# Kernel optimization log

Measured on AMD Instinct MI355X. Metric: run time of the kernel, lower is better.

## Reference

```python
import jax, jax.numpy as jnp
import numpy as np

N_NODES = 100000
N_EDGES = 300000
D = 128
HID = 128

def setup_inputs() -> dict:
    key = jax.random.key(0)
    ks = jax.random.split(key, 12)
    s = lambda fan_in: 1.0 / np.sqrt(fan_in)
    return {
        "user_emb": jax.random.normal(ks[0], (N_NODES, D), jnp.float32),
        "item_emb": jax.random.normal(ks[1], (N_NODES, D), jnp.float32),
        "ei_ui": jax.random.randint(ks[2], (2, N_EDGES), 0, N_NODES, jnp.int64),
        "ei_iu": jax.random.randint(ks[3], (2, N_EDGES), 0, N_NODES, jnp.int64),
        "W_bi_ui": jax.random.normal(ks[4], (2 * D, HID), jnp.float32) * s(2 * D),
        "b_bi_ui": jnp.zeros((HID,), jnp.float32),
        "W1_ui": jax.random.normal(ks[5], (HID, HID), jnp.float32) * s(HID),
        "b1_ui": jnp.zeros((HID,), jnp.float32),
        "W2_ui": jax.random.normal(ks[6], (HID, 1), jnp.float32) * s(HID),
        "b2_ui": jnp.zeros((1,), jnp.float32),
        "W_bi_iu": jax.random.normal(ks[7], (2 * D, HID), jnp.float32) * s(2 * D),
        "b_bi_iu": jnp.zeros((HID,), jnp.float32),
        "W1_iu": jax.random.normal(ks[8], (HID, HID), jnp.float32) * s(HID),
        "b1_iu": jnp.zeros((HID,), jnp.float32),
        "W2_iu": jax.random.normal(ks[9], (HID, 1), jnp.float32) * s(HID),
        "b2_iu": jnp.zeros((1,), jnp.float32),
    }

def _decode_edge_type(src_emb, dst_emb, edge_index, W_bi, b_bi, W1, b1, W2, b2):
    # gather endpoint embeddings and concat -> [E, 2D]
    e = jnp.concatenate([src_emb[edge_index[0]], dst_emb[edge_index[1]]], axis=1)
    h = jax.nn.elu(e @ W_bi + b_bi)          # bilinear -> ELU
    h = jax.nn.elu(h @ W1 + b1)              # linear1 -> ELU
    p = jax.nn.sigmoid(h @ W2 + b2)          # linear2 -> sigmoid
    return p.reshape(-1)                     # [E]

def reference(user_emb, item_emb, ei_ui, ei_iu,
              W_bi_ui, b_bi_ui, W1_ui, b1_ui, W2_ui, b2_ui,
              W_bi_iu, b_bi_iu, W1_iu, b1_iu, W2_iu, b2_iu):
    # edge type (user, clicks, item): source=user, target=item
    p_ui = _decode_edge_type(user_emb, item_emb, ei_ui,
                             W_bi_ui, b_bi_ui, W1_ui, b1_ui, W2_ui, b2_ui)
    # edge type (item, clicked_by, user): source=item, target=user
    p_iu = _decode_edge_type(item_emb, user_emb, ei_iu,
                             W_bi_iu, b_bi_iu, W1_iu, b1_iu, W2_iu, b2_iu)
    return jnp.stack([p_ui, p_iu])  # [2, E]
```

## Files before the change

kernel.cpp:

```cpp
#include <hip/hip_runtime.h>

typedef __attribute__((ext_vector_type(8))) short short8;
typedef __attribute__((ext_vector_type(4))) float float4v;
typedef __attribute__((ext_vector_type(4))) int int4v;

#define E_EDGES 300000
#define EPB 64
#define NBLK ((E_EDGES + EPB - 1) / EPB)
#define TAB_ELEMS 12800000

__device__ __forceinline__ short f2bf(float f) {
    unsigned u = __float_as_uint(f);
    return (short)((u + 0x7FFFu + ((u >> 16) & 1u)) >> 16);
}
__device__ __forceinline__ unsigned pk_bf16(float a, float b) {
    unsigned ua = __float_as_uint(a), ub = __float_as_uint(b);
    ua += 0x7FFFu + ((ua >> 16) & 1u);
    ub += 0x7FFFu + ((ub >> 16) & 1u);
    return __builtin_amdgcn_perm(ub, ua, 0x07060302);
}

__device__ __forceinline__ void cp16(const void* g, void* l) {
    __builtin_amdgcn_global_load_lds(
        (const __attribute__((address_space(1))) unsigned int*)g,
        (__attribute__((address_space(3))) unsigned int*)l, 16, 0, 0);
}

__global__ void prep_weights(const float* __restrict__ Wbi_ui, const float* __restrict__ W1_ui,
                             const float* __restrict__ Wbi_iu, const float* __restrict__ W1_iu,
                             short* __restrict__ ws) {
    __shared__ short tr[64 * 68];
    const int t = blockIdx.y;
    const int m = blockIdx.x;
    const float* W; int k0, n0, obase;
    if (m < 8) {
        int kt = m >> 1, nh = m & 1;
        W = t ? Wbi_iu : Wbi_ui; k0 = kt * 64; n0 = nh * 64;
        obase = t * 32768 + kt * 8192;
    } else {
        int mm = m - 8; int kt = mm >> 1, nh = mm & 1;
        W = t ? W1_iu : W1_ui; k0 = kt * 64; n0 = nh * 64;
        obase = 65536 + t * 16384 + kt * 8192;
    }
    const int tid = threadIdx.x;
    for (int it = 0; it < 16; ++it) {
        int flat = it * 256 + tid;
        int kk = flat >> 6, nn = flat & 63;
        tr[nn * 68 + kk] = f2bf(W[(size_t)(k0 + kk) * 128 + n0 + nn]);
    }
    __syncthreads();
    for (int it = 0; it < 16; ++it) {
        int flat = it * 256 + tid;
        int nn = flat >> 6, kk = flat & 63;
        int n = n0 + nn;
        ws[obase + n * 64 + (kk ^ ((n & 7) << 3))] = tr[nn * 68 + kk];
    }
}

__global__ void cvt_tables(const float* __restrict__ ue, const float* __restrict__ ie,
                           short* __restrict__ tab) {
    const float* src = blockIdx.y ? ie : ue;
    short* dst = tab + (size_t)blockIdx.y * TAB_ELEMS;
    const int stride = gridDim.x * blockDim.x;
    for (int g = blockIdx.x * blockDim.x + threadIdx.x; g < TAB_ELEMS / 8; g += stride) {
        const float* p = src + (size_t)g * 8;
        float4v v0 = ((const float4v*)p)[0];
        float4v v1 = ((const float4v*)p)[1];
        int4v w = { (int)pk_bf16(v0[0], v0[1]), (int)pk_bf16(v0[2], v0[3]),
                    (int)pk_bf16(v1[0], v1[1]), (int)pk_bf16(v1[2], v1[3]) };
        *(int4v*)(dst + (size_t)g * 8) = w;
    }
}

template<bool BF16G>
__launch_bounds__(256, 4)
__global__ void edge_decoder(
    const float* __restrict__ user_emb, const float* __restrict__ item_emb,
    const int* __restrict__ ei_ui, const int* __restrict__ ei_iu,
    const float* __restrict__ b_bi_ui, const float* __restrict__ b1_ui,
    const float* __restrict__ W2_ui, const float* __restrict__ b2_ui,
    const float* __restrict__ b_bi_iu, const float* __restrict__ b1_iu,
    const float* __restrict__ W2_iu, const float* __restrict__ b2_iu,
    const short* __restrict__ ws, const short* __restrict__ tab,
    float* __restrict__ out)
{
    __shared__ short Blds[128 * 64];
    __shared__ short Hlds[4 * 16 * 136];

    const int type = blockIdx.y;
    const int e0 = blockIdx.x * EPB;
    const int tid = threadIdx.x;
    const int wave = tid >> 6, lane = tid & 63;
    const int q = lane >> 4, ln = lane & 15;

    const int*   ei   = type ? ei_iu : ei_ui;
    const float* bbi  = type ? b_bi_iu : b_bi_ui;
    const float* b1v  = type ? b1_iu : b1_ui;
    const float* W2v  = type ? W2_iu : W2_ui;
    const float* b2v  = type ? b2_iu : b2_ui;
    const short* WbiT = ws + type * 32768;
    const short* W1T  = ws + 65536 + type * 16384;

    const int erow = e0 + wave * 16 + ln;
    const int safe = (erow < E_EDGES) ? erow : 0;
    const int si = ei[safe];
    const int di = ei[E_EDGES + safe];

    for (int c = 0; c < 4; ++c)
        cp16(WbiT + c * 2048 + tid * 8, Blds + c * 2048 + tid * 8);

    short8 a[8];
    if (BF16G) {
        const short* sp = tab + (size_t)(type ? TAB_ELEMS : 0) + (size_t)si * 128;
        const short* dp = tab + (size_t)(type ? 0 : TAB_ELEMS) + (size_t)di * 128;
        for (int ks = 0; ks < 4; ++ks)
            a[ks] = *(const short8*)(sp + ks * 32 + q * 8);
        for (int ks = 4; ks < 8; ++ks)
            a[ks] = *(const short8*)(dp + (ks - 4) * 32 + q * 8);
    } else {
        const float* srcT = type ? item_emb : user_emb;
        const float* dstT = type ? user_emb : item_emb;
        for (int ks = 0; ks < 8; ++ks) {
            const float* p = (ks < 4) ? (srcT + (size_t)si * 128 + ks * 32 + q * 8)
                                      : (dstT + (size_t)di * 128 + (ks - 4) * 32 + q * 8);
            float4v v0 = ((const float4v*)p)[0];
            float4v v1 = ((const float4v*)p)[1];
            int4v w = { (int)pk_bf16(v0[0], v0[1]), (int)pk_bf16(v0[2], v0[3]),
                        (int)pk_bf16(v1[0], v1[1]), (int)pk_bf16(v1[2], v1[3]) };
            a[ks] = *(short8*)&w;
        }
    }

    float4v acc[8];
    for (int nt = 0; nt < 8; ++nt) acc[nt] = (float4v){0.f, 0.f, 0.f, 0.f};

    const int swz = (ln & 7) << 3;

    for (int kt = 0; kt < 4; ++kt) {
        __syncthreads();
        for (int ks2 = 0; ks2 < 2; ++ks2) {
            int ka = (ks2 * 32 + q * 8) ^ swz;
            for (int nt = 0; nt < 8; ++nt) {
                short8 bf = *(const short8*)&Blds[(nt * 16 + ln) * 64 + ka];
                acc[nt] = __builtin_amdgcn_mfma_f32_16x16x32_bf16(a[kt * 2 + ks2], bf, acc[nt], 0, 0, 0);
            }
        }
        __syncthreads();
        const short* nxt = (kt < 3) ? (WbiT + (kt + 1) * 8192) : W1T;
        for (int c = 0; c < 4; ++c)
            cp16(nxt + c * 2048 + tid * 8, Blds + c * 2048 + tid * 8);
    }

    short* Hw = Hlds + wave * (16 * 136);
    for (int nt = 0; nt < 8; ++nt) {
        int col = nt * 16 + ln;
        float bb = bbi[col];
        float4v v = acc[nt];
        for (int r = 0; r < 4; ++r) {
            float x = v[r] + bb;
            float h = x > 0.f ? x : (__expf(x) - 1.f);
            Hw[(q * 4 + r) * 136 + col] = f2bf(h);
        }
    }
    short8 a2[4];
    for (int ks = 0; ks < 4; ++ks)
        a2[ks] = *(const short8*)&Hw[ln * 136 + ks * 32 + q * 8];

    for (int nt = 0; nt < 8; ++nt) acc[nt] = (float4v){0.f, 0.f, 0.f, 0.f};

    for (int kt = 0; kt < 2; ++kt) {
        __syncthreads();
        for (int ks2 = 0; ks2 < 2; ++ks2) {
            int ka = (ks2 * 32 + q * 8) ^ swz;
            for (int nt = 0; nt < 8; ++nt) {
                short8 bf = *(const short8*)&Blds[(nt * 16 + ln) * 64 + ka];
                acc[nt] = __builtin_amdgcn_mfma_f32_16x16x32_bf16(a2[kt * 2 + ks2], bf, acc[nt], 0, 0, 0);
            }
        }
        __syncthreads();
        if (kt == 0)
            for (int c = 0; c < 4; ++c)
                cp16(W1T + 8192 + c * 2048 + tid * 8, Blds + c * 2048 + tid * 8);
    }

    float s0 = 0.f, s1 = 0.f, s2 = 0.f, s3 = 0.f;
    for (int nt = 0; nt < 8; ++nt) {
        int col = nt * 16 + ln;
        float bb = b1v[col], wv = W2v[col];
        float4v v = acc[nt];
        float x;
        x = v[0] + bb; x = x > 0.f ? x : (__expf(x) - 1.f); s0 += x * wv;
        x = v[1] + bb; x = x > 0.f ? x : (__expf(x) - 1.f); s1 += x * wv;
        x = v[2] + bb; x = x > 0.f ? x : (__expf(x) - 1.f); s2 += x * wv;
        x = v[3] + bb; x = x > 0.f ? x : (__expf(x) - 1.f); s3 += x * wv;
    }
    for (int off = 1; off < 16; off <<= 1) {
        s0 += __shfl_xor(s0, off);
        s1 += __shfl_xor(s1, off);
        s2 += __shfl_xor(s2, off);
        s3 += __shfl_xor(s3, off);
    }
    if (ln < 4) {
        float sv = (ln == 0) ? s0 : (ln == 1) ? s1 : (ln == 2) ? s2 : s3;
        int e = e0 + wave * 16 + q * 4 + ln;
        if (e < E_EDGES) {
            float z = sv + b2v[0];
            out[type * E_EDGES + e] = 1.f / (1.f + __expf(-z));
        }
    }
}

extern "C" void kernel_launch(void* const* d_in, const int* in_sizes, int n_in,
                              void* d_out, int out_size, void* d_ws, size_t ws_size,
                              hipStream_t stream) {
    const float* user_emb = (const float*)d_in[0];
    const float* item_emb = (const float*)d_in[1];
    const int*   ei_ui    = (const int*)d_in[2];
    const int*   ei_iu    = (const int*)d_in[3];
    const float* W_bi_ui  = (const float*)d_in[4];
    const float* b_bi_ui  = (const float*)d_in[5];
    const float* W1_ui    = (const float*)d_in[6];
    const float* b1_ui    = (const float*)d_in[7];
    const float* W2_ui    = (const float*)d_in[8];
    const float* b2_ui    = (const float*)d_in[9];
    const float* W_bi_iu  = (const float*)d_in[10];
    const float* b_bi_iu  = (const float*)d_in[11];
    const float* W1_iu    = (const float*)d_in[12];
    const float* b1_iu    = (const float*)d_in[13];
    const float* W2_iu    = (const float*)d_in[14];
    const float* b2_iu    = (const float*)d_in[15];
    short* ws  = (short*)d_ws;
    short* tab = ws + 98304;
    float* out = (float*)d_out;

    const size_t need = 98304u * 2u + (size_t)2 * TAB_ELEMS * 2u;

    hipLaunchKernelGGL(prep_weights, dim3(12, 2), dim3(256), 0, stream,
                       W_bi_ui, W1_ui, W_bi_iu, W1_iu, ws);
    if (ws_size >= need) {
        hipLaunchKernelGGL(cvt_tables, dim3(1024, 2), dim3(256), 0, stream,
                           user_emb, item_emb, tab);
        edge_decoder<true><<<dim3(NBLK, 2), dim3(256), 0, stream>>>(
            user_emb, item_emb, ei_ui, ei_iu,
            b_bi_ui, b1_ui, W2_ui, b2_ui,
            b_bi_iu, b1_iu, W2_iu, b2_iu,
            ws, tab, out);
    } else {
        edge_decoder<false><<<dim3(NBLK, 2), dim3(256), 0, stream>>>(
            user_emb, item_emb, ei_ui, ei_iu,
            b_bi_ui, b1_ui, W2_ui, b2_ui,
            b_bi_iu, b1_iu, W2_iu, b2_iu,
            ws, tab, out);
    }
}
```

Baseline: 260.9 us.

## Process two 16-edge tiles per wave, fold biases into accumulators, merge prep kernels

Edges per block double to 128, so each wave computes two 16-row MFMA tiles. Every B fragment read from LDS is reused for both tiles, which halves LDS weight traffic and barriers per edge. Biases now seed the accumulators instead of being added in the epilogue. The weight-prep and table-conversion kernels become one launch. In exchange it needs more registers (launch bounds lowered to 3 blocks per CU) and a larger H staging buffer. The fallback path now also writes the bf16 tables into a workspace that may be too small for them.

```diff
diff --git a/kernel.cpp b/kernel.cpp
--- a/kernel.cpp
+++ b/kernel.cpp
@@ -5,7 +5,7 @@
 typedef __attribute__((ext_vector_type(4))) int int4v;
 
 #define E_EDGES 300000
-#define EPB 64
+#define EPB 128
 #define NBLK ((E_EDGES + EPB - 1) / EPB)
 #define TAB_ELEMS 12800000
 
@@ -19,19 +19,34 @@
     ub += 0x7FFFu + ((ub >> 16) & 1u);
     return __builtin_amdgcn_perm(ub, ua, 0x07060302);
 }
-
 __device__ __forceinline__ void cp16(const void* g, void* l) {
     __builtin_amdgcn_global_load_lds(
         (const __attribute__((address_space(1))) unsigned int*)g,
         (__attribute__((address_space(3))) unsigned int*)l, 16, 0, 0);
 }
 
-__global__ void prep_weights(const float* __restrict__ Wbi_ui, const float* __restrict__ W1_ui,
-                             const float* __restrict__ Wbi_iu, const float* __restrict__ W1_iu,
-                             short* __restrict__ ws) {
+__global__ void prep_all(const float* __restrict__ ue, const float* __restrict__ ie,
+                         const float* __restrict__ Wbi_ui, const float* __restrict__ W1_ui,
+                         const float* __restrict__ Wbi_iu, const float* __restrict__ W1_iu,
+                         short* __restrict__ ws) {
     __shared__ short tr[64 * 68];
     const int t = blockIdx.y;
-    const int m = blockIdx.x;
+    const int tid = threadIdx.x;
+    if (blockIdx.x < 1024) {
+        const float* src = t ? ie : ue;
+        short* dst = ws + 98304 + (size_t)t * TAB_ELEMS;
+        const int stride = 1024 * 256;
+        for (int g = blockIdx.x * 256 + tid; g < TAB_ELEMS / 8; g += stride) {
+            const float* p = src + (size_t)g * 8;
+            float4v v0 = ((const float4v*)p)[0];
+            float4v v1 = ((const float4v*)p)[1];
+            int4v w = { (int)pk_bf16(v0[0], v0[1]), (int)pk_bf16(v0[2], v0[3]),
+                        (int)pk_bf16(v1[0], v1[1]), (int)pk_bf16(v1[2], v1[3]) };
+            *(int4v*)(dst + (size_t)g * 8) = w;
+        }
+        return;
+    }
+    const int m = blockIdx.x - 1024;
     const float* W; int k0, n0, obase;
     if (m < 8) {
         int kt = m >> 1, nh = m & 1;
@@ -42,7 +57,6 @@
         W = t ? W1_iu : W1_ui; k0 = kt * 64; n0 = nh * 64;
         obase = 65536 + t * 16384 + kt * 8192;
     }
-    const int tid = threadIdx.x;
     for (int it = 0; it < 16; ++it) {
         int flat = it * 256 + tid;
         int kk = flat >> 6, nn = flat & 63;
@@ -57,23 +71,8 @@
     }
 }
 
-__global__ void cvt_tables(const float* __restrict__ ue, const float* __restrict__ ie,
-                           short* __restrict__ tab) {
-    const float* src = blockIdx.y ? ie : ue;
-    short* dst = tab + (size_t)blockIdx.y * TAB_ELEMS;
-    const int stride = gridDim.x * blockDim.x;
-    for (int g = blockIdx.x * blockDim.x + threadIdx.x; g < TAB_ELEMS / 8; g += stride) {
-        const float* p = src + (size_t)g * 8;
-        float4v v0 = ((const float4v*)p)[0];
-        float4v v1 = ((const float4v*)p)[1];
-        int4v w = { (int)pk_bf16(v0[0], v0[1]), (int)pk_bf16(v0[2], v0[3]),
-                    (int)pk_bf16(v1[0], v1[1]), (int)pk_bf16(v1[2], v1[3]) };
-        *(int4v*)(dst + (size_t)g * 8) = w;
-    }
-}
-
 template<bool BF16G>
-__launch_bounds__(256, 4)
+__launch_bounds__(256, 3)
 __global__ void edge_decoder(
     const float* __restrict__ user_emb, const float* __restrict__ item_emb,
     const int* __restrict__ ei_ui, const int* __restrict__ ei_iu,
@@ -85,7 +84,7 @@
     float* __restrict__ out)
 {
     __shared__ short Blds[128 * 64];
-    __shared__ short Hlds[4 * 16 * 136];
+    __shared__ short Hlds[4 * 32 * 136];
 
     const int type = blockIdx.y;
     const int e0 = blockIdx.x * EPB;
@@ -101,38 +100,48 @@
     const short* WbiT = ws + type * 32768;
     const short* W1T  = ws + 65536 + type * 16384;
 
-    const int erow = e0 + wave * 16 + ln;
-    const int safe = (erow < E_EDGES) ? erow : 0;
-    const int si = ei[safe];
-    const int di = ei[E_EDGES + safe];
+    int si[2], di[2];
+    for (int mt = 0; mt < 2; ++mt) {
+        int erow = e0 + wave * 32 + mt * 16 + ln;
+        int safe = (erow < E_EDGES) ? erow : 0;
+        si[mt] = ei[safe];
+        di[mt] = ei[E_EDGES + safe];
+    }
 
     for (int c = 0; c < 4; ++c)
         cp16(WbiT + c * 2048 + tid * 8, Blds + c * 2048 + tid * 8);
 
-    short8 a[8];
+    short8 a[2][8];
     if (BF16G) {
-        const short* sp = tab + (size_t)(type ? TAB_ELEMS : 0) + (size_t)si * 128;
-        const short* dp = tab + (size_t)(type ? 0 : TAB_ELEMS) + (size_t)di * 128;
-        for (int ks = 0; ks < 4; ++ks)
-            a[ks] = *(const short8*)(sp + ks * 32 + q * 8);
-        for (int ks = 4; ks < 8; ++ks)
-            a[ks] = *(const short8*)(dp + (ks - 4) * 32 + q * 8);
+        for (int mt = 0; mt < 2; ++mt) {
+            const short* sp = tab + (size_t)(type ? TAB_ELEMS : 0) + (size_t)si[mt] * 128;
+            const short* dp = tab + (size_t)(type ? 0 : TAB_ELEMS) + (size_t)di[mt] * 128;
+            for (int ks = 0; ks < 4; ++ks)
+                a[mt][ks] = *(const short8*)(sp + ks * 32 + q * 8);
+            for (int ks = 4; ks < 8; ++ks)
+                a[mt][ks] = *(const short8*)(dp + (ks - 4) * 32 + q * 8);
+        }
     } else {
         const float* srcT = type ? item_emb : user_emb;
         const float* dstT = type ? user_emb : item_emb;
-        for (int ks = 0; ks < 8; ++ks) {
-            const float* p = (ks < 4) ? (srcT + (size_t)si * 128 + ks * 32 + q * 8)
-                                      : (dstT + (size_t)di * 128 + (ks - 4) * 32 + q * 8);
-            float4v v0 = ((const float4v*)p)[0];
-            float4v v1 = ((const float4v*)p)[1];
-            int4v w = { (int)pk_bf16(v0[0], v0[1]), (int)pk_bf16(v0[2], v0[3]),
-                        (int)pk_bf16(v1[0], v1[1]), (int)pk_bf16(v1[2], v1[3]) };
-            a[ks] = *(short8*)&w;
-        }
-    }
-
-    float4v acc[8];
-    for (int nt = 0; nt < 8; ++nt) acc[nt] = (float4v){0.f, 0.f, 0.f, 0.f};
+        for (int mt = 0; mt < 2; ++mt)
+            for (int ks = 0; ks < 8; ++ks) {
+                const float* p = (ks < 4) ? (srcT + (size_t)si[mt] * 128 + ks * 32 + q * 8)
+                                          : (dstT + (size_t)di[mt] * 128 + (ks - 4) * 32 + q * 8);
+                float4v v0 = ((const float4v*)p)[0];
+                float4v v1 = ((const float4v*)p)[1];
+                int4v w = { (int)pk_bf16(v0[0], v0[1]), (int)pk_bf16(v0[2], v0[3]),
+                            (int)pk_bf16(v1[0], v1[1]), (int)pk_bf16(v1[2], v1[3]) };
+                a[mt][ks] = *(short8*)&w;
+            }
+    }
+
+    float4v acc[2][8];
+    for (int nt = 0; nt < 8; ++nt) {
+        float bb = bbi[nt * 16 + ln];
+        acc[0][nt] = (float4v){bb, bb, bb, bb};
+        acc[1][nt] = acc[0][nt];
+    }
 
     const int swz = (ln & 7) << 3;
 
@@ -140,9 +149,11 @@
         __syncthreads();
         for (int ks2 = 0; ks2 < 2; ++ks2) {
             int ka = (ks2 * 32 + q * 8) ^ swz;
+            int ks = kt * 2 + ks2;
             for (int nt = 0; nt < 8; ++nt) {
                 short8 bf = *(const short8*)&Blds[(nt * 16 + ln) * 64 + ka];
-                acc[nt] = __builtin_amdgcn_mfma_f32_16x16x32_bf16(a[kt * 2 + ks2], bf, acc[nt], 0, 0, 0);
+                acc[0][nt] = __builtin_amdgcn_mfma_f32_16x16x32_bf16(a[0][ks], bf, acc[0][nt], 0, 0, 0);
+                acc[1][nt] = __builtin_amdgcn_mfma_f32_16x16x32_bf16(a[1][ks], bf, acc[1][nt], 0, 0, 0);
             }
         }
         __syncthreads();
@@ -151,30 +162,37 @@
             cp16(nxt + c * 2048 + tid * 8, Blds + c * 2048 + tid * 8);
     }
 
-    short* Hw = Hlds + wave * (16 * 136);
+    short* Hw = Hlds + wave * (32 * 136);
+    for (int mt = 0; mt < 2; ++mt)
+        for (int nt = 0; nt < 8; ++nt) {
+            int col = nt * 16 + ln;
+            float4v v = acc[mt][nt];
+            for (int r = 0; r < 4; ++r) {
+                float x = v[r];
+                float h = x > 0.f ? x : (__expf(x) - 1.f);
+                Hw[(mt * 16 + q * 4 + r) * 136 + col] = f2bf(h);
+            }
+        }
+    short8 a2[2][4];
+    for (int mt = 0; mt < 2; ++mt)
+        for (int ks = 0; ks < 4; ++ks)
+            a2[mt][ks] = *(const short8*)&Hw[(mt * 16 + ln) * 136 + ks * 32 + q * 8];
+
     for (int nt = 0; nt < 8; ++nt) {
-        int col = nt * 16 + ln;
-        float bb = bbi[col];
-        float4v v = acc[nt];
-        for (int r = 0; r < 4; ++r) {
-            float x = v[r] + bb;
-            float h = x > 0.f ? x : (__expf(x) - 1.f);
-            Hw[(q * 4 + r) * 136 + col] = f2bf(h);
-        }
-    }
-    short8 a2[4];
-    for (int ks = 0; ks < 4; ++ks)
-        a2[ks] = *(const short8*)&Hw[ln * 136 + ks * 32 + q * 8];
-
-    for (int nt = 0; nt < 8; ++nt) acc[nt] = (float4v){0.f, 0.f, 0.f, 0.f};
+        float bb = b1v[nt * 16 + ln];
+        acc[0][nt] = (float4v){bb, bb, bb, bb};
+        acc[1][nt] = acc[0][nt];
+    }
 
     for (int kt = 0; kt < 2; ++kt) {
         __syncthreads();
         for (int ks2 = 0; ks2 < 2; ++ks2) {
             int ka = (ks2 * 32 + q * 8) ^ swz;
+            int ks = kt * 2 + ks2;
             for (int nt = 0; nt < 8; ++nt) {
                 short8 bf = *(const short8*)&Blds[(nt * 16 + ln) * 64 + ka];
-                acc[nt] = __builtin_amdgcn_mfma_f32_16x16x32_bf16(a2[kt * 2 + ks2], bf, acc[nt], 0, 0, 0);
+                acc[0][nt] = __builtin_amdgcn_mfma_f32_16x16x32_bf16(a2[0][ks], bf, acc[0][nt], 0, 0, 0);
+                acc[1][nt] = __builtin_amdgcn_mfma_f32_16x16x32_bf16(a2[1][ks], bf, acc[1][nt], 0, 0, 0);
             }
         }
         __syncthreads();
@@ -183,29 +201,30 @@
                 cp16(W1T + 8192 + c * 2048 + tid * 8, Blds + c * 2048 + tid * 8);
     }
 
-    float s0 = 0.f, s1 = 0.f, s2 = 0.f, s3 = 0.f;
-    for (int nt = 0; nt < 8; ++nt) {
-        int col = nt * 16 + ln;
-        float bb = b1v[col], wv = W2v[col];
-        float4v v = acc[nt];
-        float x;
-        x = v[0] + bb; x = x > 0.f ? x : (__expf(x) - 1.f); s0 += x * wv;
-        x = v[1] + bb; x = x > 0.f ? x : (__expf(x) - 1.f); s1 += x * wv;
-        x = v[2] + bb; x = x > 0.f ? x : (__expf(x) - 1.f); s2 += x * wv;
-        x = v[3] + bb; x = x > 0.f ? x : (__expf(x) - 1.f); s3 += x * wv;
-    }
-    for (int off = 1; off < 16; off <<= 1) {
-        s0 += __shfl_xor(s0, off);
-        s1 += __shfl_xor(s1, off);
-        s2 += __shfl_xor(s2, off);
-        s3 += __shfl_xor(s3, off);
-    }
-    if (ln < 4) {
-        float sv = (ln == 0) ? s0 : (ln == 1) ? s1 : (ln == 2) ? s2 : s3;
-        int e = e0 + wave * 16 + q * 4 + ln;
-        if (e < E_EDGES) {
-            float z = sv + b2v[0];
-            out[type * E_EDGES + e] = 1.f / (1.f + __expf(-z));
+    for (int mt = 0; mt < 2; ++mt) {
+        float s0 = 0.f, s1 = 0.f, s2 = 0.f, s3 = 0.f;
+        for (int nt = 0; nt < 8; ++nt) {
+            float wv = W2v[nt * 16 + ln];
+            float4v v = acc[mt][nt];
+            float x;
+            x = v[0]; x = x > 0.f ? x : (__expf(x) - 1.f); s0 += x * wv;
+            x = v[1]; x = x > 0.f ? x : (__expf(x) - 1.f); s1 += x * wv;
+            x = v[2]; x = x > 0.f ? x : (__expf(x) - 1.f); s2 += x * wv;
+            x = v[3]; x = x > 0.f ? x : (__expf(x) - 1.f); s3 += x * wv;
+        }
+        for (int off = 1; off < 16; off <<= 1) {
+            s0 += __shfl_xor(s0, off);
+            s1 += __shfl_xor(s1, off);
+            s2 += __shfl_xor(s2, off);
+            s3 += __shfl_xor(s3, off);
+        }
+        if (ln < 4) {
+            float sv = (ln == 0) ? s0 : (ln == 1) ? s1 : (ln == 2) ? s2 : s3;
+            int e = e0 + wave * 32 + mt * 16 + q * 4 + ln;
+            if (e < E_EDGES) {
+                float z = sv + b2v[0];
+                out[type * E_EDGES + e] = 1.f / (1.f + __expf(-z));
+            }
         }
     }
 }
@@ -235,17 +254,17 @@
 
     const size_t need = 98304u * 2u + (size_t)2 * TAB_ELEMS * 2u;
 
-    hipLaunchKernelGGL(prep_weights, dim3(12, 2), dim3(256), 0, stream,
-                       W_bi_ui, W1_ui, W_bi_iu, W1_iu, ws);
     if (ws_size >= need) {
-        hipLaunchKernelGGL(cvt_tables, dim3(1024, 2), dim3(256), 0, stream,
-                           user_emb, item_emb, tab);
+        hipLaunchKernelGGL(prep_all, dim3(1036, 2), dim3(256), 0, stream,
+                           user_emb, item_emb, W_bi_ui, W1_ui, W_bi_iu, W1_iu, ws);
         edge_decoder<true><<<dim3(NBLK, 2), dim3(256), 0, stream>>>(
             user_emb, item_emb, ei_ui, ei_iu,
             b_bi_ui, b1_ui, W2_ui, b2_ui,
             b_bi_iu, b1_iu, W2_iu, b2_iu,
             ws, tab, out);
     } else {
+        hipLaunchKernelGGL(prep_all, dim3(1036, 2), dim3(256), 0, stream,
+                           user_emb, item_emb, W_bi_ui, W1_ui, W_bi_iu, W1_iu, ws);
         edge_decoder<false><<<dim3(NBLK, 2), dim3(256), 0, stream>>>(
             user_emb, item_emb, ei_ui, ei_iu,
             b_bi_ui, b1_ui, W2_ui, b2_ui,
```

Result: faster. 250.8 us (-3.9%).
